# Kernel tuning notes

Hardware: AMD Instinct MI355X
Metric: run time of the kernel (lower is better)

Reference implementation:

```python
import jax, jax.numpy as jnp
import numpy as np

TEMPERATURE = 0.5
DIFFUSION_STEPS = 10
N = 8192
C = 128
E = 262144  # includes N self-loops to guarantee degree >= 1


def setup_inputs() -> dict:
    key = jax.random.key(0)
    k1, k2, k3, k4 = jax.random.split(key, 4)
    embeddings = jax.random.normal(k1, (N, C), dtype=jnp.float32)
    # self-loops first, then random edges
    src = jnp.concatenate([jnp.arange(N), jax.random.randint(k2, (E - N,), 0, N)])
    dst = jnp.concatenate([jnp.arange(N), jax.random.randint(k3, (E - N,), 0, N)])
    edge_index = jnp.stack([src, dst]).astype(jnp.int64)
    rand_indices = jax.random.permutation(k4, N).astype(jnp.int64)
    return {"embeddings": embeddings, "edge_index": edge_index, "rand_indices": rand_indices}


def reference(embeddings, edge_index, rand_indices):
    n = embeddings.shape[0]
    # dense adjacency via scatter-set (matches torch index assignment: duplicates -> 1)
    adj = jnp.zeros((n, n), dtype=embeddings.dtype).at[edge_index[0], edge_index[1]].set(1.0)
    d_inv_sqrt = jnp.power(adj.sum(axis=1), -0.5)  # [n]
    # D^-1/2 A D^-1/2 without materializing diag matmuls
    diffusion = d_inv_sqrt[:, None] * adj * d_inv_sqrt[None, :]
    for _ in range(DIFFUSION_STEPS):
        embeddings = diffusion @ embeddings
    pos_pairs = jnp.einsum('nc,nc->n', embeddings[edge_index[0]], embeddings[edge_index[1]]) / TEMPERATURE
    pos_loss = -jnp.mean(jax.nn.log_sigmoid(pos_pairs))
    neg_pairs = jnp.einsum('nc,nc->n', embeddings, embeddings[rand_indices]) / TEMPERATURE
    neg_loss = -jnp.mean(jax.nn.log_sigmoid(-neg_pairs))
    return pos_loss + neg_loss
```

## Files before the change

kernel.cpp:

```cpp
#include <hip/hip_runtime.h>
#include <math.h>

#define N        8192
#define C        128
#define E_TOTAL  262144
#define WPR      256
#define INV_TEMP 2.0f
#define STEPS    10
#define S_ELL    96
#define S_PAD    104
#define POS_BLOCKS 2048
#define NEG_BLOCKS 128

#define OFF_D       1024
#define OFF_CNT     (OFF_D + 32768)
#define OFF_PPOS    (OFF_CNT + 32768)
#define OFF_PNEG    (OFF_PPOS + POS_BLOCKS * 4)
#define OFF_COL     (OFF_PNEG + 512)
#define OFF_WGT     (OFF_COL + N * S_ELL * 4)
#define OFF_BITMAP  (OFF_WGT + N * S_ELL * 4)
#define BITMAP_BYTES (N * WPR * 4)
#define OFF_BUFA    OFF_BITMAP
#define OFF_BUFB    (OFF_BUFA + N * C * 2)

typedef unsigned int   uint;
typedef unsigned short ushort;

__device__ __forceinline__ float bflo(uint u) { return __uint_as_float(u << 16); }
__device__ __forceinline__ float bfhi(uint u) { return __uint_as_float(u & 0xffff0000u); }
__device__ __forceinline__ ushort f2bf(float f) {
    uint u = __float_as_uint(f);
    return (ushort)((u + 0x7fffu + ((u >> 16) & 1u)) >> 16);
}
__device__ __forceinline__ float dot_u(uint a, uint b) {
    return bflo(a) * bflo(b) + bfhi(a) * bfhi(b);
}
__device__ __forceinline__ float log_sigmoid(float z) {
    return fminf(z, 0.0f) - log1pf(expf(-fabsf(z)));
}

__global__ void scatter_edges_kernel(const int* __restrict__ ei,
                                     unsigned int* __restrict__ bm) {
    int e = blockIdx.x * blockDim.x + threadIdx.x;
    if (e >= E_TOTAL) return;
    int s = ei[e];
    int t = ei[E_TOTAL + e];
    atomicOr(&bm[s * WPR + (t >> 5)], 1u << (t & 31));
}

__global__ void degree_kernel(const unsigned int* __restrict__ bm,
                              float* __restrict__ dinv) {
    int row = blockIdx.x;
    int lane = threadIdx.x;
    const unsigned int* p = bm + row * WPR;
    int cnt = 0;
    for (int w = lane; w < WPR; w += 64) cnt += __popc(p[w]);
    for (int off = 32; off > 0; off >>= 1) cnt += __shfl_down(cnt, off, 64);
    if (lane == 0) dinv[row] = 1.0f / sqrtf((float)cnt);
}

__global__ void build_ell_kernel(const unsigned int* __restrict__ bm,
                                 const float* __restrict__ dinv,
                                 int* __restrict__ cnt,
                                 int* __restrict__ col,
                                 float* __restrict__ wgt) {
    int row = blockIdx.x;
    int lane = threadIdx.x;
    const unsigned int* p = bm + row * WPR;
    unsigned int w[4];
    int c = 0;
    for (int i = 0; i < 4; ++i) { w[i] = p[lane * 4 + i]; c += __popc(w[i]); }
    int inc = c;
    for (int off = 1; off < 64; off <<= 1) {
        int v = __shfl_up(inc, off, 64);
        if (lane >= off) inc += v;
    }
    int pos = inc - c;
    int total = __shfl(inc, 63, 64);
    float dr = dinv[row];
    for (int i = 0; i < 4; ++i) {
        unsigned int word = w[i];
        int jbase = (lane * 4 + i) << 5;
        while (word) {
            int b = __ffs(word) - 1;
            word &= word - 1;
            int j = jbase + b;
            if (pos < S_ELL) {
                col[row * S_ELL + pos] = j;
                wgt[row * S_ELL + pos] = dr * dinv[j];
            }
            ++pos;
        }
    }
    if (lane == 0) cnt[row] = (total < S_ELL) ? total : S_ELL;
}

__global__ void cvt_kernel(const float* __restrict__ x, ushort* __restrict__ y) {
    int i = blockIdx.x * blockDim.x + threadIdx.x;
    float4 v = ((const float4*)x)[i];
    ushort4 o;
    o.x = f2bf(v.x); o.y = f2bf(v.y); o.z = f2bf(v.z); o.w = f2bf(v.w);
    ((ushort4*)y)[i] = o;
}

__global__ void spmm_bf16_kernel(const int* __restrict__ cnt,
                                 const int* __restrict__ col,
                                 const float* __restrict__ wgt,
                                 const ushort* __restrict__ x,
                                 ushort* __restrict__ y) {
    __shared__ int   scol[4][S_PAD];
    __shared__ float swgt[4][S_PAD];
    int wid  = threadIdx.x >> 6;
    int lane = threadIdx.x & 63;
    int row  = blockIdx.x * 4 + wid;
    int n = cnt[row];
    int npad = (n + 7) & ~7;
    if (lane < n)      { scol[wid][lane]      = col[row * S_ELL + lane];
                         swgt[wid][lane]      = wgt[row * S_ELL + lane]; }
    if (lane + 64 < n) { scol[wid][lane + 64] = col[row * S_ELL + lane + 64];
                         swgt[wid][lane + 64] = wgt[row * S_ELL + lane + 64]; }
    if (lane < 8 && n + lane < npad) {
        scol[wid][n + lane] = row;
        swgt[wid][n + lane] = 0.0f;
    }
    __syncthreads();
    int qw  = lane >> 4;
    int l16 = lane & 15;
    float a0 = 0.f, a1 = 0.f, a2 = 0.f, a3 = 0.f;
    float a4 = 0.f, a5 = 0.f, a6 = 0.f, a7 = 0.f;
    for (int k = 0; k < npad; k += 8) {
        int   j0 = scol[wid][k + qw];      float w0 = swgt[wid][k + qw];
        int   j1 = scol[wid][k + 4 + qw];  float w1 = swgt[wid][k + 4 + qw];
        uint4 u0 = *(const uint4*)(x + j0 * C + l16 * 8);
        uint4 u1 = *(const uint4*)(x + j1 * C + l16 * 8);
        a0 += w0 * bflo(u0.x); a1 += w0 * bfhi(u0.x);
        a2 += w0 * bflo(u0.y); a3 += w0 * bfhi(u0.y);
        a4 += w0 * bflo(u0.z); a5 += w0 * bfhi(u0.z);
        a6 += w0 * bflo(u0.w); a7 += w0 * bfhi(u0.w);
        a0 += w1 * bflo(u1.x); a1 += w1 * bfhi(u1.x);
        a2 += w1 * bflo(u1.y); a3 += w1 * bfhi(u1.y);
        a4 += w1 * bflo(u1.z); a5 += w1 * bfhi(u1.z);
        a6 += w1 * bflo(u1.w); a7 += w1 * bfhi(u1.w);
    }
    a0 += __shfl_xor(a0, 16, 64); a0 += __shfl_xor(a0, 32, 64);
    a1 += __shfl_xor(a1, 16, 64); a1 += __shfl_xor(a1, 32, 64);
    a2 += __shfl_xor(a2, 16, 64); a2 += __shfl_xor(a2, 32, 64);
    a3 += __shfl_xor(a3, 16, 64); a3 += __shfl_xor(a3, 32, 64);
    a4 += __shfl_xor(a4, 16, 64); a4 += __shfl_xor(a4, 32, 64);
    a5 += __shfl_xor(a5, 16, 64); a5 += __shfl_xor(a5, 32, 64);
    a6 += __shfl_xor(a6, 16, 64); a6 += __shfl_xor(a6, 32, 64);
    a7 += __shfl_xor(a7, 16, 64); a7 += __shfl_xor(a7, 32, 64);
    if (qw == 0) {
        uint4 o;
        o.x = (uint)f2bf(a0) | ((uint)f2bf(a1) << 16);
        o.y = (uint)f2bf(a2) | ((uint)f2bf(a3) << 16);
        o.z = (uint)f2bf(a4) | ((uint)f2bf(a5) << 16);
        o.w = (uint)f2bf(a6) | ((uint)f2bf(a7) << 16);
        *(uint4*)(y + row * C + l16 * 8) = o;
    }
}

__global__ void pos_loss_kernel(const ushort* __restrict__ x,
                                const int* __restrict__ ei,
                                float* __restrict__ ppos) {
    __shared__ float wsum[4];
    int gtid = blockIdx.x * blockDim.x + threadIdx.x;
    int wave = gtid >> 6;
    int lane = threadIdx.x & 63;
    int g    = lane >> 2;
    int q    = lane & 3;
    int nwaves = (gridDim.x * blockDim.x) >> 6;
    float sum = 0.0f;
    for (int base = wave * 16; base < E_TOTAL; base += nwaves * 16) {
        int e = base + g;
        int s = ei[e];
        int t = ei[E_TOTAL + e];
        const uint4* ps = (const uint4*)(x + s * C + q * 32);
        const uint4* pt = (const uint4*)(x + t * C + q * 32);
        uint4 s0 = ps[0], s1 = ps[1], s2 = ps[2], s3 = ps[3];
        uint4 t0 = pt[0], t1 = pt[1], t2 = pt[2], t3 = pt[3];
        float p = dot_u(s0.x, t0.x) + dot_u(s0.y, t0.y) + dot_u(s0.z, t0.z) + dot_u(s0.w, t0.w)
                + dot_u(s1.x, t1.x) + dot_u(s1.y, t1.y) + dot_u(s1.z, t1.z) + dot_u(s1.w, t1.w)
                + dot_u(s2.x, t2.x) + dot_u(s2.y, t2.y) + dot_u(s2.z, t2.z) + dot_u(s2.w, t2.w)
                + dot_u(s3.x, t3.x) + dot_u(s3.y, t3.y) + dot_u(s3.z, t3.z) + dot_u(s3.w, t3.w);
        p += __shfl_xor(p, 1, 64);
        p += __shfl_xor(p, 2, 64);
        if (q == 0) sum += log_sigmoid(p * INV_TEMP);
    }
    sum += __shfl_xor(sum, 4, 64);
    sum += __shfl_xor(sum, 8, 64);
    sum += __shfl_xor(sum, 16, 64);
    sum += __shfl_xor(sum, 32, 64);
    if (lane == 0) wsum[threadIdx.x >> 6] = sum;
    __syncthreads();
    if (threadIdx.x == 0)
        ppos[blockIdx.x] = (wsum[0] + wsum[1]) + (wsum[2] + wsum[3]);
}

__global__ void neg_loss_kernel(const ushort* __restrict__ x,
                                const int* __restrict__ ridx,
                                float* __restrict__ pneg) {
    __shared__ float wsum[4];
    int gtid = blockIdx.x * blockDim.x + threadIdx.x;
    int wave = gtid >> 6;
    int lane = threadIdx.x & 63;
    int g    = lane >> 2;
    int q    = lane & 3;
    int nwaves = (gridDim.x * blockDim.x) >> 6;
    float sum = 0.0f;
    for (int base = wave * 16; base < N; base += nwaves * 16) {
        int i = base + g;
        int t = ridx[i];
        const uint4* ps = (const uint4*)(x + i * C + q * 32);
        const uint4* pt = (const uint4*)(x + t * C + q * 32);
        uint4 s0 = ps[0], s1 = ps[1], s2 = ps[2], s3 = ps[3];
        uint4 t0 = pt[0], t1 = pt[1], t2 = pt[2], t3 = pt[3];
        float p = dot_u(s0.x, t0.x) + dot_u(s0.y, t0.y) + dot_u(s0.z, t0.z) + dot_u(s0.w, t0.w)
                + dot_u(s1.x, t1.x) + dot_u(s1.y, t1.y) + dot_u(s1.z, t1.z) + dot_u(s1.w, t1.w)
                + dot_u(s2.x, t2.x) + dot_u(s2.y, t2.y) + dot_u(s2.z, t2.z) + dot_u(s2.w, t2.w)
                + dot_u(s3.x, t3.x) + dot_u(s3.y, t3.y) + dot_u(s3.z, t3.z) + dot_u(s3.w, t3.w);
        p += __shfl_xor(p, 1, 64);
        p += __shfl_xor(p, 2, 64);
        if (q == 0) sum += log_sigmoid(-p * INV_TEMP);
    }
    sum += __shfl_xor(sum, 4, 64);
    sum += __shfl_xor(sum, 8, 64);
    sum += __shfl_xor(sum, 16, 64);
    sum += __shfl_xor(sum, 32, 64);
    if (lane == 0) wsum[threadIdx.x >> 6] = sum;
    __syncthreads();
    if (threadIdx.x == 0)
        pneg[blockIdx.x] = (wsum[0] + wsum[1]) + (wsum[2] + wsum[3]);
}

__global__ void finalize_kernel(const float* __restrict__ ppos,
                                const float* __restrict__ pneg,
                                float* __restrict__ out) {
    __shared__ float red[256];
    int t = threadIdx.x;
    float s = 0.0f;
    for (int i = t; i < POS_BLOCKS; i += 256) s += ppos[i];
    float sn = (t < NEG_BLOCKS) ? pneg[t] : 0.0f;
    red[t] = s * (-1.0f / (float)E_TOTAL) + sn * (-1.0f / (float)N);
    __syncthreads();
    for (int off = 128; off > 0; off >>= 1) {
        if (t < off) red[t] += red[t + off];
        __syncthreads();
    }
    if (t == 0) out[0] = red[0];
}

extern "C" void kernel_launch(void* const* d_in, const int* in_sizes, int n_in,
                              void* d_out, int out_size, void* d_ws, size_t ws_size,
                              hipStream_t stream) {
    (void)in_sizes; (void)n_in; (void)out_size; (void)ws_size;

    const float* emb_in = (const float*)d_in[0];
    const int*   ei     = (const int*)d_in[1];
    const int*   ridx   = (const int*)d_in[2];
    float* out = (float*)d_out;

    char* ws = (char*)d_ws;
    float*        dinv = (float*)(ws + OFF_D);
    int*          cnt  = (int*)(ws + OFF_CNT);
    float*        ppos = (float*)(ws + OFF_PPOS);
    float*        pneg = (float*)(ws + OFF_PNEG);
    int*          col  = (int*)(ws + OFF_COL);
    float*        wgt  = (float*)(ws + OFF_WGT);
    unsigned int* bm   = (unsigned int*)(ws + OFF_BITMAP);
    ushort*       bufA = (ushort*)(ws + OFF_BUFA);
    ushort*       bufB = (ushort*)(ws + OFF_BUFB);
    ushort*       buf[2] = {bufA, bufB};

    hipMemsetAsync(bm, 0, BITMAP_BYTES, stream);

    scatter_edges_kernel<<<E_TOTAL / 256, 256, 0, stream>>>(ei, bm);
    degree_kernel<<<N, 64, 0, stream>>>(bm, dinv);
    build_ell_kernel<<<N, 64, 0, stream>>>(bm, dinv, cnt, col, wgt);

    cvt_kernel<<<(N * C / 4) / 256, 256, 0, stream>>>(emb_in, bufA);

    for (int s = 0; s < STEPS; ++s) {
        const ushort* xs = buf[s & 1];
        ushort* yd = buf[(s + 1) & 1];
        spmm_bf16_kernel<<<N / 4, 256, 0, stream>>>(cnt, col, wgt, xs, yd);
    }
    const ushort* emb = buf[STEPS & 1];

    pos_loss_kernel<<<POS_BLOCKS, 256, 0, stream>>>(emb, ei, ppos);
    neg_loss_kernel<<<NEG_BLOCKS, 256, 0, stream>>>(emb, ridx, pneg);
    finalize_kernel<<<1, 256, 0, stream>>>(ppos, pneg, out);
}
```

Before: 185.4 us.

## Interleave ELL col/weight, drop LDS staging, fuse convert into first SpMM and merge loss kernels

```diff
diff --git a/kernel.cpp b/kernel.cpp
--- a/kernel.cpp
+++ b/kernel.cpp
@@ -16,9 +16,8 @@
 #define OFF_CNT     (OFF_D + 32768)
 #define OFF_PPOS    (OFF_CNT + 32768)
 #define OFF_PNEG    (OFF_PPOS + POS_BLOCKS * 4)
-#define OFF_COL     (OFF_PNEG + 512)
-#define OFF_WGT     (OFF_COL + N * S_ELL * 4)
-#define OFF_BITMAP  (OFF_WGT + N * S_ELL * 4)
+#define OFF_ELL     (OFF_PNEG + 1024)
+#define OFF_BITMAP  (OFF_ELL + N * S_PAD * 8)
 #define BITMAP_BYTES (N * WPR * 4)
 #define OFF_BUFA    OFF_BITMAP
 #define OFF_BUFB    (OFF_BUFA + N * C * 2)
@@ -62,8 +61,7 @@
 __global__ void build_ell_kernel(const unsigned int* __restrict__ bm,
                                  const float* __restrict__ dinv,
                                  int* __restrict__ cnt,
-                                 int* __restrict__ col,
-                                 float* __restrict__ wgt) {
+                                 int2* __restrict__ ell) {
     int row = blockIdx.x;
     int lane = threadIdx.x;
     const unsigned int* p = bm + row * WPR;
@@ -78,6 +76,7 @@
     int pos = inc - c;
     int total = __shfl(inc, 63, 64);
     float dr = dinv[row];
+    int2* er = ell + row * S_PAD;
     for (int i = 0; i < 4; ++i) {
         unsigned int word = w[i];
         int jbase = (lane * 4 + i) << 5;
@@ -86,61 +85,70 @@
             word &= word - 1;
             int j = jbase + b;
             if (pos < S_ELL) {
-                col[row * S_ELL + pos] = j;
-                wgt[row * S_ELL + pos] = dr * dinv[j];
+                int2 pr; pr.x = j; pr.y = __float_as_int(dr * dinv[j]);
+                er[pos] = pr;
             }
             ++pos;
         }
     }
-    if (lane == 0) cnt[row] = (total < S_ELL) ? total : S_ELL;
-}
-
-__global__ void cvt_kernel(const float* __restrict__ x, ushort* __restrict__ y) {
-    int i = blockIdx.x * blockDim.x + threadIdx.x;
-    float4 v = ((const float4*)x)[i];
-    ushort4 o;
-    o.x = f2bf(v.x); o.y = f2bf(v.y); o.z = f2bf(v.z); o.w = f2bf(v.w);
-    ((ushort4*)y)[i] = o;
-}
-
-__global__ void spmm_bf16_kernel(const int* __restrict__ cnt,
-                                 const int* __restrict__ col,
-                                 const float* __restrict__ wgt,
-                                 const ushort* __restrict__ x,
-                                 ushort* __restrict__ y) {
-    __shared__ int   scol[4][S_PAD];
-    __shared__ float swgt[4][S_PAD];
+    int ncap = (total < S_ELL) ? total : S_ELL;
+    int npad = (ncap + 7) & ~7;
+    if (lane < npad - ncap) {
+        int2 pr; pr.x = row; pr.y = 0;
+        er[ncap + lane] = pr;
+    }
+    if (lane == 0) cnt[row] = npad;
+}
+
+__global__ __launch_bounds__(256) void spmm_step_kernel(
+        const int* __restrict__ cnt,
+        const int2* __restrict__ ell,
+        const void* __restrict__ xin,
+        ushort* __restrict__ y,
+        int first) {
     int wid  = threadIdx.x >> 6;
     int lane = threadIdx.x & 63;
     int row  = blockIdx.x * 4 + wid;
-    int n = cnt[row];
-    int npad = (n + 7) & ~7;
-    if (lane < n)      { scol[wid][lane]      = col[row * S_ELL + lane];
-                         swgt[wid][lane]      = wgt[row * S_ELL + lane]; }
-    if (lane + 64 < n) { scol[wid][lane + 64] = col[row * S_ELL + lane + 64];
-                         swgt[wid][lane + 64] = wgt[row * S_ELL + lane + 64]; }
-    if (lane < 8 && n + lane < npad) {
-        scol[wid][n + lane] = row;
-        swgt[wid][n + lane] = 0.0f;
-    }
-    __syncthreads();
-    int qw  = lane >> 4;
-    int l16 = lane & 15;
+    int npad = cnt[row];
+    int qw   = lane >> 4;
+    int l16  = lane & 15;
+    const int2* er = ell + row * S_PAD;
     float a0 = 0.f, a1 = 0.f, a2 = 0.f, a3 = 0.f;
     float a4 = 0.f, a5 = 0.f, a6 = 0.f, a7 = 0.f;
-    for (int k = 0; k < npad; k += 8) {
-        int   j0 = scol[wid][k + qw];      float w0 = swgt[wid][k + qw];
-        int   j1 = scol[wid][k + 4 + qw];  float w1 = swgt[wid][k + 4 + qw];
-        uint4 u0 = *(const uint4*)(x + j0 * C + l16 * 8);
-        uint4 u1 = *(const uint4*)(x + j1 * C + l16 * 8);
-        a0 += w0 * bflo(u0.x); a1 += w0 * bfhi(u0.x);
-        a2 += w0 * bflo(u0.y); a3 += w0 * bfhi(u0.y);
-        a4 += w0 * bflo(u0.z); a5 += w0 * bfhi(u0.z);
-        a6 += w0 * bflo(u0.w); a7 += w0 * bfhi(u0.w);
-        a0 += w1 * bflo(u1.x); a1 += w1 * bfhi(u1.x);
-        a2 += w1 * bflo(u1.y); a3 += w1 * bfhi(u1.y);
-        a4 += w1 * bflo(u1.z); a5 += w1 * bfhi(u1.z);
-        a6 += w1 * bflo(u1.w); a7 += w1 * bfhi(u1.w);
+    if (first) {
+        const float* x = (const float*)xin;
+        for (int k = 0; k < npad; k += 8) {
+            int2 p0 = er[k + qw];
+            int2 p1 = er[k + 4 + qw];
+            float w0 = __int_as_float(p0.y);
+            float w1 = __int_as_float(p1.y);
+            const float* r0 = x + p0.x * C + l16 * 8;
+            const float* r1 = x + p1.x * C + l16 * 8;
+            float4 u0a = *(const float4*)r0, u0b = *(const float4*)(r0 + 4);
+            float4 u1a = *(const float4*)r1, u1b = *(const float4*)(r1 + 4);
+            a0 += w0 * u0a.x; a1 += w0 * u0a.y; a2 += w0 * u0a.z; a3 += w0 * u0a.w;
+            a4 += w0 * u0b.x; a5 += w0 * u0b.y; a6 += w0 * u0b.z; a7 += w0 * u0b.w;
+            a0 += w1 * u1a.x; a1 += w1 * u1a.y; a2 += w1 * u1a.z; a3 += w1 * u1a.w;
+            a4 += w1 * u1b.x; a5 += w1 * u1b.y; a6 += w1 * u1b.z; a7 += w1 * u1b.w;
+        }
+    } else {
+        const ushort* x = (const ushort*)xin;
+        for (int k = 0; k < npad; k += 8) {
+            int2 p0 = er[k + qw];
+            int2 p1 = er[k + 4 + qw];
+            float w0 = __int_as_float(p0.y);
+            float w1 = __int_as_float(p1.y);
+            uint4 u0 = *(const uint4*)(x + p0.x * C + l16 * 8);
+            uint4 u1 = *(const uint4*)(x + p1.x * C + l16 * 8);
+            a0 += w0 * bflo(u0.x); a1 += w0 * bfhi(u0.x);
+            a2 += w0 * bflo(u0.y); a3 += w0 * bfhi(u0.y);
+            a4 += w0 * bflo(u0.z); a5 += w0 * bfhi(u0.z);
+            a6 += w0 * bflo(u0.w); a7 += w0 * bfhi(u0.w);
+            a0 += w1 * bflo(u1.x); a1 += w1 * bfhi(u1.x);
+            a2 += w1 * bflo(u1.y); a3 += w1 * bfhi(u1.y);
+            a4 += w1 * bflo(u1.z); a5 += w1 * bfhi(u1.z);
+            a6 += w1 * bflo(u1.w); a7 += w1 * bfhi(u1.w);
+        }
     }
     a0 += __shfl_xor(a0, 16, 64); a0 += __shfl_xor(a0, 32, 64);
     a1 += __shfl_xor(a1, 16, 64); a1 += __shfl_xor(a1, 32, 64);
@@ -160,32 +168,54 @@
     }
 }
 
-__global__ void pos_loss_kernel(const ushort* __restrict__ x,
-                                const int* __restrict__ ei,
-                                float* __restrict__ ppos) {
+__global__ void loss_kernel(const ushort* __restrict__ x,
+                            const int* __restrict__ ei,
+                            const int* __restrict__ ridx,
+                            float* __restrict__ ppos,
+                            float* __restrict__ pneg) {
     __shared__ float wsum[4];
-    int gtid = blockIdx.x * blockDim.x + threadIdx.x;
-    int wave = gtid >> 6;
     int lane = threadIdx.x & 63;
     int g    = lane >> 2;
     int q    = lane & 3;
-    int nwaves = (gridDim.x * blockDim.x) >> 6;
     float sum = 0.0f;
-    for (int base = wave * 16; base < E_TOTAL; base += nwaves * 16) {
-        int e = base + g;
-        int s = ei[e];
-        int t = ei[E_TOTAL + e];
-        const uint4* ps = (const uint4*)(x + s * C + q * 32);
-        const uint4* pt = (const uint4*)(x + t * C + q * 32);
-        uint4 s0 = ps[0], s1 = ps[1], s2 = ps[2], s3 = ps[3];
-        uint4 t0 = pt[0], t1 = pt[1], t2 = pt[2], t3 = pt[3];
-        float p = dot_u(s0.x, t0.x) + dot_u(s0.y, t0.y) + dot_u(s0.z, t0.z) + dot_u(s0.w, t0.w)
-                + dot_u(s1.x, t1.x) + dot_u(s1.y, t1.y) + dot_u(s1.z, t1.z) + dot_u(s1.w, t1.w)
-                + dot_u(s2.x, t2.x) + dot_u(s2.y, t2.y) + dot_u(s2.z, t2.z) + dot_u(s2.w, t2.w)
-                + dot_u(s3.x, t3.x) + dot_u(s3.y, t3.y) + dot_u(s3.z, t3.z) + dot_u(s3.w, t3.w);
-        p += __shfl_xor(p, 1, 64);
-        p += __shfl_xor(p, 2, 64);
-        if (q == 0) sum += log_sigmoid(p * INV_TEMP);
+    if (blockIdx.x < POS_BLOCKS) {
+        int wave = (blockIdx.x * blockDim.x + threadIdx.x) >> 6;
+        int nwaves = (POS_BLOCKS * 256) >> 6;
+        for (int base = wave * 16; base < E_TOTAL; base += nwaves * 16) {
+            int e = base + g;
+            int s = ei[e];
+            int t = ei[E_TOTAL + e];
+            const uint4* ps = (const uint4*)(x + s * C + q * 32);
+            const uint4* pt = (const uint4*)(x + t * C + q * 32);
+            uint4 s0 = ps[0], s1 = ps[1], s2 = ps[2], s3 = ps[3];
+            uint4 t0 = pt[0], t1 = pt[1], t2 = pt[2], t3 = pt[3];
+            float p = dot_u(s0.x, t0.x) + dot_u(s0.y, t0.y) + dot_u(s0.z, t0.z) + dot_u(s0.w, t0.w)
+                    + dot_u(s1.x, t1.x) + dot_u(s1.y, t1.y) + dot_u(s1.z, t1.z) + dot_u(s1.w, t1.w)
+                    + dot_u(s2.x, t2.x) + dot_u(s2.y, t2.y) + dot_u(s2.z, t2.z) + dot_u(s2.w, t2.w)
+                    + dot_u(s3.x, t3.x) + dot_u(s3.y, t3.y) + dot_u(s3.z, t3.z) + dot_u(s3.w, t3.w);
+            p += __shfl_xor(p, 1, 64);
+            p += __shfl_xor(p, 2, 64);
+            if (q == 0) sum += log_sigmoid(p * INV_TEMP);
+        }
+    } else {
+        int bi = blockIdx.x - POS_BLOCKS;
+        int wave = (bi * blockDim.x + threadIdx.x) >> 6;
+        int nwaves = (NEG_BLOCKS * 256) >> 6;
+        for (int base = wave * 16; base < N; base += nwaves * 16) {
+            int i = base + g;
+            int t = ridx[i];
+            const uint4* ps = (const uint4*)(x + i * C + q * 32);
+            const uint4* pt = (const uint4*)(x + t * C + q * 32);
+            uint4 s0 = ps[0], s1 = ps[1], s2 = ps[2], s3 = ps[3];
+            uint4 t0 = pt[0], t1 = pt[1], t2 = pt[2], t3 = pt[3];
+            float p = dot_u(s0.x, t0.x) + dot_u(s0.y, t0.y) + dot_u(s0.z, t0.z) + dot_u(s0.w, t0.w)
+                    + dot_u(s1.x, t1.x) + dot_u(s1.y, t1.y) + dot_u(s1.z, t1.z) + dot_u(s1.w, t1.w)
+                    + dot_u(s2.x, t2.x) + dot_u(s2.y, t2.y) + dot_u(s2.z, t2.z) + dot_u(s2.w, t2.w)
+                    + dot_u(s3.x, t3.x) + dot_u(s3.y, t3.y) + dot_u(s3.z, t3.z) + dot_u(s3.w, t3.w);
+            p += __shfl_xor(p, 1, 64);
+            p += __shfl_xor(p, 2, 64);
+            if (q == 0) sum += log_sigmoid(-p * INV_TEMP);
+        }
     }
     sum += __shfl_xor(sum, 4, 64);
     sum += __shfl_xor(sum, 8, 64);
@@ -193,44 +223,11 @@
     sum += __shfl_xor(sum, 32, 64);
     if (lane == 0) wsum[threadIdx.x >> 6] = sum;
     __syncthreads();
-    if (threadIdx.x == 0)
-        ppos[blockIdx.x] = (wsum[0] + wsum[1]) + (wsum[2] + wsum[3]);
-}
-
-__global__ void neg_loss_kernel(const ushort* __restrict__ x,
-                                const int* __restrict__ ridx,
-                                float* __restrict__ pneg) {
-    __shared__ float wsum[4];
-    int gtid = blockIdx.x * blockDim.x + threadIdx.x;
-    int wave = gtid >> 6;
-    int lane = threadIdx.x & 63;
-    int g    = lane >> 2;
-    int q    = lane & 3;
-    int nwaves = (gridDim.x * blockDim.x) >> 6;
-    float sum = 0.0f;
-    for (int base = wave * 16; base < N; base += nwaves * 16) {
-        int i = base + g;
-        int t = ridx[i];
-        const uint4* ps = (const uint4*)(x + i * C + q * 32);
-        const uint4* pt = (const uint4*)(x + t * C + q * 32);
-        uint4 s0 = ps[0], s1 = ps[1], s2 = ps[2], s3 = ps[3];
-        uint4 t0 = pt[0], t1 = pt[1], t2 = pt[2], t3 = pt[3];
-        float p = dot_u(s0.x, t0.x) + dot_u(s0.y, t0.y) + dot_u(s0.z, t0.z) + dot_u(s0.w, t0.w)
-                + dot_u(s1.x, t1.x) + dot_u(s1.y, t1.y) + dot_u(s1.z, t1.z) + dot_u(s1.w, t1.w)
-                + dot_u(s2.x, t2.x) + dot_u(s2.y, t2.y) + dot_u(s2.z, t2.z) + dot_u(s2.w, t2.w)
-                + dot_u(s3.x, t3.x) + dot_u(s3.y, t3.y) + dot_u(s3.z, t3.z) + dot_u(s3.w, t3.w);
-        p += __shfl_xor(p, 1, 64);
-        p += __shfl_xor(p, 2, 64);
-        if (q == 0) sum += log_sigmoid(-p * INV_TEMP);
-    }
-    sum += __shfl_xor(sum, 4, 64);
-    sum += __shfl_xor(sum, 8, 64);
-    sum += __shfl_xor(sum, 16, 64);
-    sum += __shfl_xor(sum, 32, 64);
-    if (lane == 0) wsum[threadIdx.x >> 6] = sum;
-    __syncthreads();
-    if (threadIdx.x == 0)
-        pneg[blockIdx.x] = (wsum[0] + wsum[1]) + (wsum[2] + wsum[3]);
+    if (threadIdx.x == 0) {
+        float v = (wsum[0] + wsum[1]) + (wsum[2] + wsum[3]);
+        if (blockIdx.x < POS_BLOCKS) ppos[blockIdx.x] = v;
+        else                         pneg[blockIdx.x - POS_BLOCKS] = v;
+    }
 }
 
 __global__ void finalize_kernel(const float* __restrict__ ppos,
@@ -265,8 +262,7 @@
     int*          cnt  = (int*)(ws + OFF_CNT);
     float*        ppos = (float*)(ws + OFF_PPOS);
     float*        pneg = (float*)(ws + OFF_PNEG);
-    int*          col  = (int*)(ws + OFF_COL);
-    float*        wgt  = (float*)(ws + OFF_WGT);
+    int2*         ell  = (int2*)(ws + OFF_ELL);
     unsigned int* bm   = (unsigned int*)(ws + OFF_BITMAP);
     ushort*       bufA = (ushort*)(ws + OFF_BUFA);
     ushort*       bufB = (ushort*)(ws + OFF_BUFB);
@@ -276,18 +272,15 @@
 
     scatter_edges_kernel<<<E_TOTAL / 256, 256, 0, stream>>>(ei, bm);
     degree_kernel<<<N, 64, 0, stream>>>(bm, dinv);
-    build_ell_kernel<<<N, 64, 0, stream>>>(bm, dinv, cnt, col, wgt);
-
-    cvt_kernel<<<(N * C / 4) / 256, 256, 0, stream>>>(emb_in, bufA);
+    build_ell_kernel<<<N, 64, 0, stream>>>(bm, dinv, cnt, ell);
 
     for (int s = 0; s < STEPS; ++s) {
-        const ushort* xs = buf[s & 1];
+        const void* xs = (s == 0) ? (const void*)emb_in : (const void*)buf[s & 1];
         ushort* yd = buf[(s + 1) & 1];
-        spmm_bf16_kernel<<<N / 4, 256, 0, stream>>>(cnt, col, wgt, xs, yd);
+        spmm_step_kernel<<<N / 4, 256, 0, stream>>>(cnt, ell, xs, yd, s == 0 ? 1 : 0);
     }
     const ushort* emb = buf[STEPS & 1];
 
-    pos_loss_kernel<<<POS_BLOCKS, 256, 0, stream>>>(emb, ei, ppos);
-    neg_loss_kernel<<<NEG_BLOCKS, 256, 0, stream>>>(emb, ridx, pneg);
+    loss_kernel<<<POS_BLOCKS + NEG_BLOCKS, 256, 0, stream>>>(emb, ei, ridx, ppos, pneg);
     finalize_kernel<<<1, 256, 0, stream>>>(ppos, pneg, out);
 }
```

Result: slower. 191.0 us (+3.0%).
